# Optimization experiments

Measured on AMD Instinct MI355X. Metric: run time of the kernel, lower is better.

Reference implementation:

```python
import jax, jax.numpy as jnp
import numpy as np

MIN_DELAY = 60
MAX_DELAY = 420
TAU = 0.0          # module's self.tau (min magnitude for resonant_activation)
TEMPERATURE = 1.0  # forward() default gumbel-softmax temperature


def setup_inputs() -> dict:
    key = jax.random.key(0)
    k1, k2, k3, k4 = jax.random.split(key, 4)
    B, T = 128, 8192
    excitation = jax.random.normal(k1, (B, 1, T), dtype=jnp.float32)
    u = jax.random.uniform(k2, (MAX_DELAY - MIN_DELAY,), dtype=jnp.float32,
                           minval=1e-6, maxval=1.0 - 1e-6)
    gumbel_noise = -jnp.log(-jnp.log(u))  # standard Gumbel samples
    delay_param = jax.random.normal(k3, (MAX_DELAY - MIN_DELAY,), dtype=jnp.float32)
    feedback_gain = jnp.ones((1,), dtype=jnp.float32)
    reflection_coeffs = jax.random.normal(k4, (2,), dtype=jnp.float32)
    return {"excitation": excitation, "gumbel_noise": gumbel_noise,
            "delay_param": delay_param, "feedback_gain": feedback_gain,
            "reflection_coeffs": reflection_coeffs}


def _resonant_activation(x, min_magnitude):
    sign = jnp.sign(x)
    magnitude = jnp.abs(jnp.tanh(x))
    return sign * (min_magnitude + (1.0 - min_magnitude) * magnitude)


def _build_coeffs(gumbel_noise, delay_param, feedback_gain, reflection_coeffs):
    # gumbel_softmax(tau=TEMPERATURE, hard=True) with straight-through estimator
    logits = (delay_param + gumbel_noise) / TEMPERATURE
    soft = jax.nn.softmax(logits)
    hard = jax.nn.one_hot(jnp.argmax(soft), soft.shape[0], dtype=soft.dtype)
    one_hot = jax.lax.stop_gradient(hard - soft) + soft
    shifted = jnp.roll(one_hot, 1)
    # low_pass_bias=False -> tanh, then resonant_activation (applies tanh again, as in source)
    rc = jnp.tanh(reflection_coeffs)
    k1 = _resonant_activation(rc[0], TAU)
    k2 = _resonant_activation(rc[1], TAU)
    a1 = k1 * (1.0 - k2)
    a2 = jnp.clip(k2, -0.999, 0.999)
    a1_bound = 0.999 - jnp.abs(a2)
    a1 = jnp.clip(a1, -a1_bound, a1_bound)
    g = jax.nn.sigmoid(feedback_gain[0]) ** 0.45
    a1 = a1 * g
    a2 = a2 * g
    tail = one_hot * a1 + shifted * a2               # [max_delay - min_delay]
    coeffs = jnp.concatenate([jnp.zeros((MIN_DELAY,), tail.dtype), tail])  # [max_delay]
    return coeffs


def _sample_wise_lpc(x, coeffs):
    # All-pole IIR: y[t] = x[t] - sum_{i=0}^{D-1} coeffs[i] * y[t-1-i]
    B, T = x.shape
    D = coeffs.shape[0]
    buf0 = jnp.zeros((B, D), x.dtype)  # buf[:, i] = y[t-1-i]

    def step(buf, x_t):
        y_t = x_t - buf @ coeffs                              # [B]
        buf = jnp.concatenate([y_t[:, None], buf[:, :-1]], 1)  # shift delay line
        return buf, y_t

    _, ys = jax.lax.scan(step, buf0, x.T)  # ys: [T, B]
    return ys.T


def reference(excitation, gumbel_noise, delay_param, feedback_gain, reflection_coeffs):
    coeffs = _build_coeffs(gumbel_noise, delay_param, feedback_gain, reflection_coeffs)
    x = excitation[:, 0, :]                 # [B, T]
    y = _sample_wise_lpc(x, coeffs)         # [B, T]
    return y[:, None, :]                    # [B, 1, T]
```

## Files before the change

kernel.cpp:

```cpp
#include <hip/hip_runtime.h>
#include <cmath>

#define T_LEN 8192
#define B_ROWS 128
#define ND 360
#define MIN_DELAY_C 60
#define BLOCK 1024
#define GSTRIDE (4 * BLOCK)


template<int NT, bool MASK>
__device__ __forceinline__ void fir_group(const float* __restrict__ src,
                                          float* __restrict__ dst, int t0,
                                          const float* __restrict__ c,
                                          const int* __restrict__ l)
{
    const float4 x = *(const float4*)&src[t0];
    float r[NT][4];
#pragma unroll
    for (int j = 0; j < NT; ++j) {
#pragma unroll
        for (int e = 0; e < 4; ++e) {
            const int s = t0 + e - l[j];
            if (MASK) {
                const float v = src[(s >= 0) ? s : 0];
                r[j][e] = (s >= 0) ? v : 0.0f;
            } else {
                r[j][e] = src[s];
            }
        }
    }
    float acc[4] = {x.x, x.y, x.z, x.w};
#pragma unroll
    for (int j = 0; j < NT; ++j)
#pragma unroll
        for (int e = 0; e < 4; ++e) acc[e] += c[j] * r[j][e];
    *(float4*)&dst[t0] = make_float4(acc[0], acc[1], acc[2], acc[3]);
}

__global__ __launch_bounds__(BLOCK) void ks_resonator_kernel(
    const float* __restrict__ excitation,
    const float* __restrict__ gumbel,
    const float* __restrict__ delay_param,
    const float* __restrict__ feedback_gain,
    const float* __restrict__ refl,
    float* __restrict__ out)
{
    __shared__ __align__(16) float bufA[T_LEN];
    __shared__ __align__(16) float bufB[T_LEN];
    __shared__ float s_c1[2], s_c2[3], s_c4[5], s_c8[9];
    __shared__ int   s_l1[2], s_l2[3], s_l4[5], s_l8[9];
    __shared__ int   s_dA, s_dB;

    const int tid = threadIdx.x;
    const int row = blockIdx.x;

    if (tid < 960) {
        const float4* __restrict__ x4 = (const float4*)(excitation + (size_t)row * T_LEN);
        float4* a4 = (float4*)bufA;
        for (int i = tid; i < T_LEN / 4; i += 960) a4[i] = x4[i];
    } else {
        const int lane = tid - 960;
        float v = -INFINITY; int idx = 0;
        for (int i = lane; i < ND; i += 64) {
            float w = delay_param[i] + gumbel[i];
            if (w > v) { v = w; idx = i; }
        }
#pragma unroll
        for (int off = 32; off > 0; off >>= 1) {
            float v2 = __shfl_xor(v, off);
            int   i2 = __shfl_xor(idx, off);
            if (v2 > v || (v2 == v && i2 < idx)) { v = v2; idx = i2; }
        }
        if (lane == 0) {
            const int p = idx;
            float k1 = tanhf(tanhf(refl[0]));
            float k2 = tanhf(tanhf(refl[1]));
            float a1 = k1 * (1.0f - k2);
            float a2 = fminf(fmaxf(k2, -0.999f), 0.999f);
            float bound = 0.999f - fabsf(a2);
            a1 = fminf(fmaxf(a1, -bound), bound);
            float fg = feedback_gain[0];
            float g = powf(1.0f / (1.0f + expf(-fg)), 0.45f);
            a1 *= g; a2 *= g;
            const int p2 = (p + 1) % ND;
            const int dA = MIN_DELAY_C + p + 1;
            const int dB = MIN_DELAY_C + p2 + 1;

            float p1[9], q2[9];
            p1[0] = 1.0f; q2[0] = 1.0f;
            for (int i = 1; i < 9; ++i) { p1[i] = p1[i-1] * a1; q2[i] = q2[i-1] * a2; }
            const float C2[3] = {1.f, 2.f, 1.f};
            const float C4[5] = {1.f, 4.f, 6.f, 4.f, 1.f};
            const float C8[9] = {1.f, 8.f, 28.f, 56.f, 70.f, 56.f, 28.f, 8.f, 1.f};
            s_c1[0] = -a1; s_l1[0] = dA;
            s_c1[1] = -a2; s_l1[1] = dB;
            for (int i = 0; i < 3; ++i) { s_c2[i] = C2[i] * p1[i] * q2[2-i]; s_l2[i] = i*dA + (2-i)*dB; }
            for (int i = 0; i < 5; ++i) { s_c4[i] = C4[i] * p1[i] * q2[4-i]; s_l4[i] = i*dA + (4-i)*dB; }
            for (int i = 0; i < 9; ++i) { s_c8[i] = C8[i] * p1[i] * q2[8-i]; s_l8[i] = i*dA + (8-i)*dB; }
            s_dA = dA; s_dB = dB;
        }
    }
    __syncthreads();

    const int t0 = 4 * tid;
    const int t1 = t0 + GSTRIDE;

    {
        float c[2]; int l[2];
#pragma unroll
        for (int j = 0; j < 2; ++j) { c[j] = s_c1[j]; l[j] = s_l1[j]; }
        fir_group<2, true >(bufA, bufB, t0, c, l);
        fir_group<2, false>(bufA, bufB, t1, c, l);
    }
    __syncthreads();

    {
        float c[3]; int l[3];
#pragma unroll
        for (int j = 0; j < 3; ++j) { c[j] = s_c2[j]; l[j] = s_l2[j]; }
        fir_group<3, true >(bufB, bufA, t0, c, l);
        fir_group<3, false>(bufB, bufA, t1, c, l);
    }
    __syncthreads();

    {
        float c[5]; int l[5];
#pragma unroll
        for (int j = 0; j < 5; ++j) { c[j] = s_c4[j]; l[j] = s_l4[j]; }
        fir_group<5, true >(bufA, bufB, t0, c, l);
        fir_group<5, false>(bufA, bufB, t1, c, l);
    }
    __syncthreads();

    {
        float c[9]; int l[9];
#pragma unroll
        for (int j = 0; j < 9; ++j) { c[j] = s_c8[j]; l[j] = s_l8[j]; }
        const int dA = s_dA, dB = s_dB;
        const int dmin = (dA < dB) ? dA : dB;
        const int W = 8 * dmin;
        for (int pos = 0; pos < T_LEN; pos += W) {
            int end = pos + W; if (end > T_LEN) end = T_LEN;
            for (int j = pos + tid; j < end; j += BLOCK) {
                float r[10];
                r[0] = bufB[j];
#pragma unroll
                for (int k = 0; k < 9; ++k) {
                    const int s = j - l[k];
                    const float v = bufB[(s >= 0) ? s : 0];
                    r[k + 1] = (s >= 0) ? v : 0.0f;
                }
                float acc = r[0];
#pragma unroll
                for (int k = 0; k < 9; ++k) acc += c[k] * r[k + 1];
                bufB[j] = acc;
            }
            __syncthreads();
        }
    }

    float4* __restrict__ o4 = (float4*)(out + (size_t)row * T_LEN);
    const float4* b4 = (const float4*)bufB;
    for (int i = tid; i < T_LEN / 4; i += BLOCK) o4[i] = b4[i];
}

extern "C" void kernel_launch(void* const* d_in, const int* in_sizes, int n_in,
                              void* d_out, int out_size, void* d_ws, size_t ws_size,
                              hipStream_t stream) {
    const float* excitation    = (const float*)d_in[0];
    const float* gumbel        = (const float*)d_in[1];
    const float* delay_param   = (const float*)d_in[2];
    const float* feedback_gain = (const float*)d_in[3];
    const float* refl          = (const float*)d_in[4];
    float* out = (float*)d_out;

    ks_resonator_kernel<<<B_ROWS, BLOCK, 0, stream>>>(
        excitation, gumbel, delay_param, feedback_gain, refl, out);
}
```

Before: 74.48 us.

## Keep FIR center values in registers and stream output directly to global

The FIR stages now use a strided per-thread element layout (tid + k*BLOCK) and keep each thread's running center value in registers across stages, so the center is no longer re-read from LDS. The first window of the final recursive stage is identical to the stage-3 output, so it is written to global straight away and the recursion starts at W. This also drops one barrier. Later windows write to global as they are computed, which replaces the final LDS-to-global copy. The cost is scalar instead of float4 LDS accesses and scalar global stores inside the sequential window loop.

```diff
diff --git a/kernel.cpp b/kernel.cpp
--- a/kernel.cpp
+++ b/kernel.cpp
@@ -6,36 +6,42 @@
 #define ND 360
 #define MIN_DELAY_C 60
 #define BLOCK 1024
-#define GSTRIDE (4 * BLOCK)
+#define NCH 8
 
 
-template<int NT, bool MASK>
-__device__ __forceinline__ void fir_group(const float* __restrict__ src,
-                                          float* __restrict__ dst, int t0,
-                                          const float* __restrict__ c,
-                                          const int* __restrict__ l)
+template<int NT, int K0, bool MASK, bool STORE>
+__device__ __forceinline__ void fir_quad(const float* __restrict__ src,
+                                         float* __restrict__ dst,
+                                         float* __restrict__ cen,
+                                         const float* __restrict__ c,
+                                         const int* __restrict__ l,
+                                         int tid, float* __restrict__ gout, int W)
 {
-    const float4 x = *(const float4*)&src[t0];
-    float r[NT][4];
+    float r[4][NT];
 #pragma unroll
-    for (int j = 0; j < NT; ++j) {
+    for (int u = 0; u < 4; ++u) {
+        const int t = tid + (K0 + u) * BLOCK;
 #pragma unroll
-        for (int e = 0; e < 4; ++e) {
-            const int s = t0 + e - l[j];
+        for (int j = 0; j < NT; ++j) {
+            const int s = t - l[j];
             if (MASK) {
                 const float v = src[(s >= 0) ? s : 0];
-                r[j][e] = (s >= 0) ? v : 0.0f;
+                r[u][j] = (s >= 0) ? v : 0.0f;
             } else {
-                r[j][e] = src[s];
+                r[u][j] = src[s];
             }
         }
     }
-    float acc[4] = {x.x, x.y, x.z, x.w};
 #pragma unroll
-    for (int j = 0; j < NT; ++j)
+    for (int u = 0; u < 4; ++u) {
+        const int t = tid + (K0 + u) * BLOCK;
+        float acc = cen[K0 + u];
 #pragma unroll
-        for (int e = 0; e < 4; ++e) acc[e] += c[j] * r[j][e];
-    *(float4*)&dst[t0] = make_float4(acc[0], acc[1], acc[2], acc[3]);
+        for (int j = 0; j < NT; ++j) acc += c[j] * r[u][j];
+        cen[K0 + u] = acc;
+        dst[t] = acc;
+        if (STORE) { if (t < W) gout[t] = acc; }
+    }
 }
 
 __global__ __launch_bounds__(BLOCK) void ks_resonator_kernel(
@@ -50,7 +56,7 @@
     __shared__ __align__(16) float bufB[T_LEN];
     __shared__ float s_c1[2], s_c2[3], s_c4[5], s_c8[9];
     __shared__ int   s_l1[2], s_l2[3], s_l4[5], s_l8[9];
-    __shared__ int   s_dA, s_dB;
+    __shared__ int   s_dmin;
 
     const int tid = threadIdx.x;
     const int row = blockIdx.x;
@@ -98,20 +104,24 @@
             for (int i = 0; i < 3; ++i) { s_c2[i] = C2[i] * p1[i] * q2[2-i]; s_l2[i] = i*dA + (2-i)*dB; }
             for (int i = 0; i < 5; ++i) { s_c4[i] = C4[i] * p1[i] * q2[4-i]; s_l4[i] = i*dA + (4-i)*dB; }
             for (int i = 0; i < 9; ++i) { s_c8[i] = C8[i] * p1[i] * q2[8-i]; s_l8[i] = i*dA + (8-i)*dB; }
-            s_dA = dA; s_dB = dB;
+            s_dmin = (dA < dB) ? dA : dB;
         }
     }
     __syncthreads();
 
-    const int t0 = 4 * tid;
-    const int t1 = t0 + GSTRIDE;
+    float* __restrict__ o = out + (size_t)row * T_LEN;
+    const int W = 8 * s_dmin;
+
+    float cen[NCH];
+#pragma unroll
+    for (int k = 0; k < NCH; ++k) cen[k] = bufA[tid + k * BLOCK];
 
     {
         float c[2]; int l[2];
 #pragma unroll
         for (int j = 0; j < 2; ++j) { c[j] = s_c1[j]; l[j] = s_l1[j]; }
-        fir_group<2, true >(bufA, bufB, t0, c, l);
-        fir_group<2, false>(bufA, bufB, t1, c, l);
+        fir_quad<2, 0, true , false>(bufA, bufB, cen, c, l, tid, nullptr, 0);
+        fir_quad<2, 4, false, false>(bufA, bufB, cen, c, l, tid, nullptr, 0);
     }
     __syncthreads();
 
@@ -119,8 +129,8 @@
         float c[3]; int l[3];
 #pragma unroll
         for (int j = 0; j < 3; ++j) { c[j] = s_c2[j]; l[j] = s_l2[j]; }
-        fir_group<3, true >(bufB, bufA, t0, c, l);
-        fir_group<3, false>(bufB, bufA, t1, c, l);
+        fir_quad<3, 0, true , false>(bufB, bufA, cen, c, l, tid, nullptr, 0);
+        fir_quad<3, 4, false, false>(bufB, bufA, cen, c, l, tid, nullptr, 0);
     }
     __syncthreads();
 
@@ -128,41 +138,33 @@
         float c[5]; int l[5];
 #pragma unroll
         for (int j = 0; j < 5; ++j) { c[j] = s_c4[j]; l[j] = s_l4[j]; }
-        fir_group<5, true >(bufA, bufB, t0, c, l);
-        fir_group<5, false>(bufA, bufB, t1, c, l);
+        fir_quad<5, 0, true , true >(bufA, bufB, cen, c, l, tid, o, W);
+        fir_quad<5, 4, false, true >(bufA, bufB, cen, c, l, tid, o, W);
     }
-    __syncthreads();
 
     {
         float c[9]; int l[9];
 #pragma unroll
         for (int j = 0; j < 9; ++j) { c[j] = s_c8[j]; l[j] = s_l8[j]; }
-        const int dA = s_dA, dB = s_dB;
-        const int dmin = (dA < dB) ? dA : dB;
-        const int W = 8 * dmin;
-        for (int pos = 0; pos < T_LEN; pos += W) {
+        for (int pos = W; pos < T_LEN; pos += W) {
+            __syncthreads();
             int end = pos + W; if (end > T_LEN) end = T_LEN;
             for (int j = pos + tid; j < end; j += BLOCK) {
-                float r[10];
-                r[0] = bufB[j];
+                float r[9];
 #pragma unroll
                 for (int k = 0; k < 9; ++k) {
                     const int s = j - l[k];
                     const float v = bufB[(s >= 0) ? s : 0];
-                    r[k + 1] = (s >= 0) ? v : 0.0f;
+                    r[k] = (s >= 0) ? v : 0.0f;
                 }
-                float acc = r[0];
+                float acc = bufB[j];
 #pragma unroll
-                for (int k = 0; k < 9; ++k) acc += c[k] * r[k + 1];
+                for (int k = 0; k < 9; ++k) acc += c[k] * r[k];
                 bufB[j] = acc;
+                o[j] = acc;
             }
-            __syncthreads();
         }
     }
-
-    float4* __restrict__ o4 = (float4*)(out + (size_t)row * T_LEN);
-    const float4* b4 = (const float4*)bufB;
-    for (int i = tid; i < T_LEN / 4; i += BLOCK) o4[i] = b4[i];
 }
 
 extern "C" void kernel_launch(void* const* d_in, const int* in_sizes, int n_in,
```

Result: faster. 71.23 us (-4.4%).
